# Performance work log

Measured on AMD Instinct MI355X. Metric: run time of the kernel, lower is better.

Reference implementation:

```python
import jax, jax.numpy as jnp
import numpy as np

NUM_HEADS = 16
NUM_KV_HEADS = 8
HEAD_DIM = 128
HIDDEN = 2048
Q_SIZE = NUM_HEADS * HEAD_DIM          # 2048
KV_SIZE = NUM_KV_HEADS * HEAD_DIM      # 1024
SCALING = 256.0 ** -0.5                # query_pre_attn_scalar ** -0.5
EPS = 1e-6
BATCH = 8
ENC_LEN = 512                          # encoder_len_per_req
Q_LEN = 2048                           # sum of extend_seq_lens (8 * 256)
KV_LEN = BATCH * ENC_LEN               # 4096


def _rms_norm(x, w):
    # Gemma3RMSNorm: fp32 compute, scale by (1 + weight)
    xf = x.astype(jnp.float32)
    xf = xf * jax.lax.rsqrt(jnp.mean(xf * xf, axis=-1, keepdims=True) + EPS)
    return (xf * (1.0 + w.astype(jnp.float32))).astype(x.dtype)


def setup_inputs() -> dict:
    key = jax.random.key(0)
    k1, k2, k3 = jax.random.split(key, 3)
    return {
        "hidden_states": jax.random.normal(k1, (Q_LEN, HIDDEN), jnp.float32),
        "encoder_hidden_states": jax.random.normal(k2, (KV_LEN, HIDDEN), jnp.float32),
        "w_qkv": jax.random.normal(k3, (Q_SIZE + 2 * KV_SIZE, HIDDEN), jnp.float32) * 0.02,
        "q_norm_w": jnp.zeros((HEAD_DIM,), jnp.float32),
        "k_norm_w": jnp.zeros((HEAD_DIM,), jnp.float32),
        "seq_lens": jnp.full((BATCH,), Q_LEN // BATCH, jnp.int32),  # extend_seq_lens per request
    }


def reference(hidden_states, encoder_hidden_states, w_qkv, q_norm_w, k_norm_w, seq_lens):
    # decoder side: only q is used
    qkv_dec = hidden_states @ w_qkv.T                     # [q_len, 4096]
    q = qkv_dec[:, :Q_SIZE].reshape(Q_LEN, NUM_HEADS, HEAD_DIM)
    q = _rms_norm(q, q_norm_w) * SCALING

    # encoder side: only k, v are used
    qkv_enc = encoder_hidden_states @ w_qkv.T             # [kv_len, 4096]
    k = qkv_enc[:, Q_SIZE:Q_SIZE + KV_SIZE].reshape(KV_LEN, NUM_KV_HEADS, HEAD_DIM)
    v = qkv_enc[:, Q_SIZE + KV_SIZE:].reshape(KV_LEN, NUM_KV_HEADS, HEAD_DIM)
    k = _rms_norm(k, k_norm_w)

    # GQA: repeat each kv head n_rep times (consecutively, matching expand+reshape)
    n_rep = NUM_HEADS // NUM_KV_HEADS
    k = jnp.repeat(k, n_rep, axis=1)                      # [kv_len, H, D]
    v = jnp.repeat(v, n_rep, axis=1)

    # scores per head: [H, q_len, kv_len]
    scores = jnp.einsum('qhd,khd->hqk', q, k)

    # ragged block-diagonal mask: query token i belongs to request r iff
    # cumsum(seq_lens)[r-1] <= i < cumsum(seq_lens)[r]; kv token j -> j // ENC_LEN
    q_req = jnp.searchsorted(jnp.cumsum(seq_lens), jnp.arange(Q_LEN), side='right')
    kv_req = jnp.arange(KV_LEN) // ENC_LEN
    mask = q_req[:, None] == kv_req[None, :]              # [q_len, kv_len] bool
    scores = jnp.where(mask[None, :, :], scores, -jnp.inf)

    attn = jax.nn.softmax(scores.astype(jnp.float32), axis=-1).astype(v.dtype)
    out = jnp.einsum('hqk,khd->qhd', attn, v)             # [q_len, H, D]
    return out.reshape(Q_LEN, NUM_HEADS * HEAD_DIM)
```

## Files before the change

kernel.cpp:

```cpp
#include <hip/hip_runtime.h>

typedef __attribute__((ext_vector_type(8))) short short8;
typedef __attribute__((ext_vector_type(4))) float f32x4;

#define DEVI __device__ __forceinline__

static constexpr int HIDDEN   = 2048;
static constexpr int NHEADS   = 16;
static constexpr int NKV      = 8;
static constexpr int HDIM     = 128;
static constexpr int QLEN     = 2048;
static constexpr int KVLEN    = 4096;
static constexpr int ENCLEN   = 512;
static constexpr int NREQ     = 8;
static constexpr float SCALING = 0.0625f;
static constexpr float EPS     = 1e-6f;

DEVI unsigned short f2bf(float f) {
  unsigned int b = __float_as_uint(f);
  b += 0x7FFFu + ((b >> 16) & 1u);
  return (unsigned short)(b >> 16);
}

DEVI void g2l16(const void* g, void* l) {
  __builtin_amdgcn_global_load_lds(
      (const __attribute__((address_space(1))) void*)g,
      (__attribute__((address_space(3))) void*)l, 16, 0, 0);
}

__global__ __launch_bounds__(256) void cvt_all(const float* __restrict__ h,
                                               const float* __restrict__ e,
                                               const float* __restrict__ w,
                                               unsigned short* __restrict__ hb,
                                               unsigned short* __restrict__ eb,
                                               unsigned short* __restrict__ wb) {
  constexpr long S1 = (long)2048 * 2048, S2 = (long)4096 * 2048;
  long i = ((long)blockIdx.x * 256 + threadIdx.x) * 8;
  const float* src;
  unsigned short* dst;
  if (i < S1)           { src = h + i;            dst = hb + i; }
  else if (i < S1 + S2) { src = e + (i - S1);     dst = eb + (i - S1); }
  else                  { src = w + (i - S1 - S2); dst = wb + (i - S1 - S2); }
  float4 a = *(const float4*)src;
  float4 b = *(const float4*)(src + 4);
  short8 o;
  o[0] = (short)f2bf(a.x); o[1] = (short)f2bf(a.y);
  o[2] = (short)f2bf(a.z); o[3] = (short)f2bf(a.w);
  o[4] = (short)f2bf(b.x); o[5] = (short)f2bf(b.y);
  o[6] = (short)f2bf(b.z); o[7] = (short)f2bf(b.w);
  *(short8*)dst = o;
}


#define SBAR  __builtin_amdgcn_s_barrier()

DEVI short8 rdfrag(const char* unit, int row, int lg) {
  int L = row >> 1;
  int g = ((row & 1) << 2) + lg;
  return *(const short8*)(unit + L * 128 + ((g ^ (L & 7)) << 4));
}

__global__ __launch_bounds__(512, 2) void gemm_qkv8(
    const unsigned short* __restrict__ Adec, const unsigned short* __restrict__ Aenc,
    const unsigned short* __restrict__ Bw,
    const float* __restrict__ q_nw, const float* __restrict__ k_nw,
    unsigned short* __restrict__ q_bf, unsigned short* __restrict__ k_bf,
    unsigned short* __restrict__ v_t) {
  extern __shared__ char lds[];
  const int K = 2048, NST = 64;

  int flat = blockIdx.y * 8 + blockIdx.x;
  int swz = (flat & 7) * 24 + (flat >> 3);
  int bx = swz & 7, by = swz >> 3;

  const unsigned short* A;
  int bm0;
  if (by < 8) { A = Adec; bm0 = by * 256; }
  else        { A = Aenc; bm0 = (by - 8) * 256; }
  const unsigned short* Bp = Bw + (by < 8 ? 0 : (size_t)2048 * 2048);
  const int bn0 = bx * 256;

  const int tid = threadIdx.x, lane = tid & 63, wave = tid >> 6;
  const int lr = lane & 15, lg = lane >> 4;
  const int wr = wave >> 2, wc = wave & 3;
  const int bq = (wc & 1) * 64;

  const int sB = tid * 16;
  const int sL = sB >> 7, sgp = (sB >> 4) & 7;
  const int sg = sgp ^ (sL & 7);
  const int st_row = sL * 2 + (sg >> 2);
  const int st_col = (sg & 3) * 8;
  const size_t a0off = (size_t)(bm0 + st_row) * K + st_col;
  const size_t a1off = a0off + (size_t)128 * K;
  const size_t b0off = (size_t)(bn0 + st_row) * K + st_col;
  const size_t b1off = b0off + (size_t)128 * K;

#define STG4(t)                                                       \
  {                                                                   \
    const size_t kc = (size_t)(t) * 32;                               \
    char* base = lds + ((t) % 3) * 32768;                             \
    g2l16(A + a0off + kc,  base + sB);                                \
    g2l16(A + a1off + kc,  base + 8192 + sB);                         \
    g2l16(Bp + b0off + kc, base + 16384 + sB);                        \
    g2l16(Bp + b1off + kc, base + 24576 + sB);                        \
  }

  f32x4 acc[8][4] = {};

#define MM(mq, aS, bS)                                                \
  {                                                                   \
    __builtin_amdgcn_s_setprio(1);                                    \
    _Pragma("unroll") for (int m = 0; m < 4; ++m)                     \
        _Pragma("unroll") for (int n = 0; n < 4; ++n)                 \
            acc[(mq)*4 + m][n] = __builtin_amdgcn_mfma_f32_16x16x32_bf16( \
                aS[m], bS[n], acc[(mq)*4 + m][n], 0, 0, 0);           \
    __builtin_amdgcn_s_setprio(0);                                    \
  }

  STG4(0); STG4(1);

#pragma unroll 3
  for (int t = 0; t < NST - 1; ++t) {
    asm volatile("s_waitcnt vmcnt(4)" ::: "memory");
    SBAR;
    const char* ua = lds + (t % 3) * 32768 + wr * 8192;
    const char* ub = lds + (t % 3) * 32768 + 16384 + ((wc >> 1) << 13);
    short8 a0[4], b0[4], a1[4];
#pragma unroll
    for (int m = 0; m < 4; ++m) a0[m] = rdfrag(ua, m * 16 + lr, lg);
#pragma unroll
    for (int n = 0; n < 4; ++n) b0[n] = rdfrag(ub, bq + n * 16 + lr, lg);
    if (t < NST - 2) STG4(t + 2);
    MM(0, a0, b0);
#pragma unroll
    for (int m = 0; m < 4; ++m) a1[m] = rdfrag(ua, 64 + m * 16 + lr, lg);
    MM(1, a1, b0);
  }
  {
    asm volatile("s_waitcnt vmcnt(0)" ::: "memory");
    SBAR;
    const char* ua = lds + ((NST - 1) % 3) * 32768 + wr * 8192;
    const char* ub = lds + ((NST - 1) % 3) * 32768 + 16384 + ((wc >> 1) << 13);
    short8 a0[4], b0[4], a1[4];
#pragma unroll
    for (int m = 0; m < 4; ++m) a0[m] = rdfrag(ua, m * 16 + lr, lg);
#pragma unroll
    for (int n = 0; n < 4; ++n) b0[n] = rdfrag(ub, bq + n * 16 + lr, lg);
    MM(0, a0, b0);
#pragma unroll
    for (int m = 0; m < 4; ++m) a1[m] = rdfrag(ua, 64 + m * 16 + lr, lg);
    MM(1, a1, b0);
  }

  const int btype = (by < 8) ? 0 : (bx < 4 ? 1 : 2);
  const int tokbase0 = (by < 8 ? by : by - 8) * 256;

  if (btype < 2) {
    float* Lf = (float*)lds;
    const float* wnorm = (btype == 0) ? q_nw : k_nw;
    const float fscale = (btype == 0) ? SCALING : 1.0f;
    unsigned short* dst = (btype == 0) ? q_bf : k_bf;
    const size_t LEN = (btype == 0) ? (size_t)QLEN : (size_t)KVLEN;
    const int dloc = lr * 8;
    float wv[8];
#pragma unroll
    for (int j = 0; j < 8; ++j) wv[j] = 1.0f + wnorm[dloc + j];

#pragma unroll
    for (int q = 0; q < 4; ++q) {
      SBAR;
      if (wr == (q >> 1)) {
        const int amb = (q & 1) * 4;
#pragma unroll
        for (int am2 = 0; am2 < 4; ++am2)
#pragma unroll
          for (int n = 0; n < 4; ++n)
#pragma unroll
            for (int r = 0; r < 4; ++r)
              Lf[(am2 * 16 + lg * 4 + r) * 260 + wc * 64 + n * 16 + lr] =
                  acc[amb + am2][n][r];
      }
      SBAR;
#pragma unroll
      for (int it = 0; it < 4; ++it) {
        int pair = it * 32 + wave * 4 + (lane >> 4);
        int row = pair >> 1, hh = pair & 1;
        const float* src = &Lf[row * 260 + hh * 128 + dloc];
        f32x4 x0 = *(const f32x4*)src;
        f32x4 x1 = *(const f32x4*)(src + 4);
        float ssq = x0[0]*x0[0] + x0[1]*x0[1] + x0[2]*x0[2] + x0[3]*x0[3] +
                    x1[0]*x1[0] + x1[1]*x1[1] + x1[2]*x1[2] + x1[3]*x1[3];
#pragma unroll
        for (int m = 8; m >= 1; m >>= 1) ssq += __shfl_xor(ssq, m);
        float sc = rsqrtf(ssq * (1.0f / 128.0f) + EPS) * fscale;
        short8 o;
        o[0] = (short)f2bf(x0[0] * sc * wv[0]); o[1] = (short)f2bf(x0[1] * sc * wv[1]);
        o[2] = (short)f2bf(x0[2] * sc * wv[2]); o[3] = (short)f2bf(x0[3] * sc * wv[3]);
        o[4] = (short)f2bf(x1[0] * sc * wv[4]); o[5] = (short)f2bf(x1[1] * sc * wv[5]);
        o[6] = (short)f2bf(x1[2] * sc * wv[6]); o[7] = (short)f2bf(x1[3] * sc * wv[7]);
        int tok = tokbase0 + q * 64 + row;
        int hd = 2 * bx + hh;
        *(short8*)&dst[((size_t)hd * LEN + tok) * 128 + dloc] = o;
      }
    }
  } else {
    float* Lv = (float*)lds;
#pragma unroll
    for (int q = 0; q < 4; ++q) {
      SBAR;
      if (wr == (q >> 1)) {
        const int amb = (q & 1) * 4;
#pragma unroll
        for (int am2 = 0; am2 < 4; ++am2)
#pragma unroll
          for (int n = 0; n < 4; ++n)
            *(f32x4*)&Lv[(wc * 64 + n * 16 + lr) * 68 + am2 * 16 + lg * 4] =
                acc[amb + am2][n];
      }
      SBAR;
      int d = tid >> 1, th = tid & 1;
      const float* src = &Lv[d * 68 + th * 32];
      int kh = (bx - 4) * 2 + (d >> 7);
      int tok = tokbase0 + q * 64 + th * 32;
      unsigned short* vp = &v_t[((size_t)kh * 128 + (d & 127)) * KVLEN + tok];
#pragma unroll
      for (int j = 0; j < 4; ++j) {
        f32x4 v0 = *(const f32x4*)(src + j * 8);
        f32x4 v1 = *(const f32x4*)(src + j * 8 + 4);
        short8 o;
        o[0] = (short)f2bf(v0[0]); o[1] = (short)f2bf(v0[1]);
        o[2] = (short)f2bf(v0[2]); o[3] = (short)f2bf(v0[3]);
        o[4] = (short)f2bf(v1[0]); o[5] = (short)f2bf(v1[1]);
        o[6] = (short)f2bf(v1[2]); o[7] = (short)f2bf(v1[3]);
        *(short8*)(vp + j * 8) = o;
      }
    }
  }
#undef STG4
#undef MM
}

__global__ __launch_bounds__(256, 4) void attn_kernel(
    const unsigned short* __restrict__ qb,
    const unsigned short* __restrict__ kb,
    const unsigned short* __restrict__ vt,
    const int* __restrict__ seq_lens,
    float* __restrict__ out) {
  __shared__ __align__(16) char smem[73728];

  const int h = blockIdx.y;
  const int t0 = blockIdx.x * 64;
  int req = 0, qs = 0;
#pragma unroll 1
  while (req < NREQ - 1 && qs + seq_lens[req] <= t0) { qs += seq_lens[req]; ++req; }
  const int slen = seq_lens[req];
  const int rows = min(64, qs + slen - t0);
  if (rows <= 0) return;
  const int qbase = t0;

  const int tid = threadIdx.x, lane = tid & 63, wave = tid >> 6;
  const int lr = lane & 15, lg = lane >> 4;
  const int m0w = wave * 16;
  const int kh = h >> 1;
  const int kv0 = req * ENCLEN;

#define STAGE_K(c, db)                                                        \
  _Pragma("unroll") for (int i = 0; i < 4; ++i) {                             \
    int idx = i * 256 + tid;                                                  \
    int row = idx >> 4, slot = idx & 15;                                      \
    g2l16(kb + ((size_t)kh * KVLEN + kv0 + (c) * 64 + row) * 128 +            \
              ((slot ^ (row & 15)) << 3),                                     \
          smem + (db) * 16384 + idx * 16);                                    \
  }
#define STAGE_V(c, db)                                                        \
  _Pragma("unroll") for (int i = 0; i < 4; ++i) {                             \
    int idx = i * 256 + tid;                                                  \
    int row = idx >> 3, slot = idx & 7;                                       \
    g2l16(vt + ((size_t)kh * 128 + row) * KVLEN + kv0 + (c) * 64 +            \
              ((slot ^ (row & 7)) << 3),                                      \
          smem + 32768 + (db) * 16384 + idx * 16);                            \
  }

  unsigned short* Ps = (unsigned short*)(smem + 65536);

  short8 a_q[4];
  {
    int qr = qbase + min(m0w + lr, rows - 1);
    const unsigned short* qp = qb + ((size_t)h * QLEN + qr) * 128 + lg * 8;
#pragma unroll
    for (int ks = 0; ks < 4; ++ks) a_q[ks] = *(const short8*)(qp + ks * 32);
  }

  f32x4 acc[8] = {};
  float mrow[4], lsum[4];
#pragma unroll
  for (int r = 0; r < 4; ++r) { mrow[r] = -1e30f; lsum[r] = 0.f; }

  STAGE_K(0, 0); STAGE_V(0, 0);

  int cb = 0;
#pragma unroll 1
  for (int c = 0; c < 8; ++c) {
    asm volatile("s_waitcnt vmcnt(0)" ::: "memory");
    __syncthreads();
    if (c < 7) { STAGE_K(c + 1, cb ^ 1); STAGE_V(c + 1, cb ^ 1); }
    const unsigned short* Kb = (const unsigned short*)(smem + cb * 16384);
    const unsigned short* Vb = (const unsigned short*)(smem + 32768 + cb * 16384);

    f32x4 s[4] = {};
#pragma unroll
    for (int ks = 0; ks < 4; ++ks) {
      short8 bk[4];
#pragma unroll
      for (int n = 0; n < 4; ++n) {
        int row = n * 16 + lr;
        bk[n] = *(const short8*)&Kb[row * 128 + (((ks * 4 + lg) ^ (row & 15)) << 3)];
      }
#pragma unroll
      for (int n = 0; n < 4; ++n)
        s[n] = __builtin_amdgcn_mfma_f32_16x16x32_bf16(a_q[ks], bk[n], s[n], 0, 0, 0);
    }

#pragma unroll
    for (int r = 0; r < 4; ++r) {
      float mx = fmaxf(fmaxf(s[0][r], s[1][r]), fmaxf(s[2][r], s[3][r]));
#pragma unroll
      for (int msk = 8; msk >= 1; msk >>= 1) mx = fmaxf(mx, __shfl_xor(mx, msk));
      float mnew = fmaxf(mrow[r], mx);
      float al = __expf(mrow[r] - mnew);
      mrow[r] = mnew;
      float rs = 0.f;
#pragma unroll
      for (int n = 0; n < 4; ++n) {
        float p = __expf(s[n][r] - mnew);
        s[n][r] = p;
        rs += p;
      }
#pragma unroll
      for (int msk = 8; msk >= 1; msk >>= 1) rs += __shfl_xor(rs, msk);
      lsum[r] = lsum[r] * al + rs;
#pragma unroll
      for (int n2 = 0; n2 < 8; ++n2) acc[n2][r] *= al;
    }

#pragma unroll
    for (int n = 0; n < 4; ++n)
#pragma unroll
      for (int r = 0; r < 4; ++r) {
        int row = m0w + lg * 4 + r;
        int col = n * 16 + lr;
        Ps[row * 64 + (col ^ ((row & 7) << 3))] = f2bf(s[n][r]);
      }
    asm volatile("s_waitcnt lgkmcnt(0)" ::: "memory");
    __builtin_amdgcn_sched_barrier(0);

#pragma unroll
    for (int ks = 0; ks < 2; ++ks) {
      int prow = m0w + lr;
      short8 pa = *(const short8*)&Ps[prow * 64 + (((ks * 4 + lg) ^ (prow & 7)) << 3)];
#pragma unroll
      for (int n2 = 0; n2 < 8; ++n2) {
        int row = n2 * 16 + lr;
        short8 bv = *(const short8*)&Vb[row * 64 + (((ks * 4 + lg) ^ (row & 7)) << 3)];
        acc[n2] = __builtin_amdgcn_mfma_f32_16x16x32_bf16(pa, bv, acc[n2], 0, 0, 0);
      }
    }
    cb ^= 1;
  }
  __syncthreads();

  float inv[4];
#pragma unroll
  for (int r = 0; r < 4; ++r) inv[r] = 1.0f / lsum[r];
#pragma unroll
  for (int n2 = 0; n2 < 8; ++n2)
#pragma unroll
    for (int r = 0; r < 4; ++r) acc[n2][r] *= inv[r];

  constexpr int OFS = 132;
  float* Of = (float*)smem;
#pragma unroll
  for (int n2 = 0; n2 < 8; ++n2)
#pragma unroll
    for (int r = 0; r < 4; ++r)
      Of[(m0w + lg * 4 + r) * OFS + n2 * 16 + lr] = acc[n2][r];
  __syncthreads();
#pragma unroll
  for (int p = 0; p < 8; ++p) {
    int idx = p * 256 + tid;
    int row = idx >> 5, c4 = (idx & 31) * 4;
    if (row < rows) {
      f32x4 v = *(const f32x4*)&Of[row * OFS + c4];
      *(f32x4*)&out[(size_t)(qbase + row) * 2048 + h * 128 + c4] = v;
    }
  }
#undef STAGE_K
#undef STAGE_V
}

extern "C" void kernel_launch(void* const* d_in, const int* in_sizes, int n_in,
                              void* d_out, int out_size, void* d_ws, size_t ws_size,
                              hipStream_t stream) {
  const float* hidden = (const float*)d_in[0];
  const float* enc    = (const float*)d_in[1];
  const float* w_qkv  = (const float*)d_in[2];
  const float* q_nw   = (const float*)d_in[3];
  const float* k_nw   = (const float*)d_in[4];
  const int*   slens  = (const int*)d_in[5];
  float* out = (float*)d_out;

  char* ws = (char*)d_ws;
  unsigned short* h_bf = (unsigned short*)(ws + 0);
  unsigned short* e_bf = (unsigned short*)(ws + 8388608);
  unsigned short* w_bf = (unsigned short*)(ws + 25165824);
  unsigned short* q_bf = (unsigned short*)(ws + 41943040);
  unsigned short* k_bf = (unsigned short*)(ws + 50331648);
  unsigned short* v_t  = (unsigned short*)(ws + 58720256);

  static bool attr_set = false;
  if (!attr_set) {
    hipFuncSetAttribute((const void*)gemm_qkv8,
                        hipFuncAttributeMaxDynamicSharedMemorySize, 131072);
    attr_set = true;
  }

  cvt_all<<<10240, 256, 0, stream>>>(hidden, enc, w_qkv, h_bf, e_bf, w_bf);

  gemm_qkv8<<<dim3(8, 24), 512, 131072, stream>>>(h_bf, e_bf, w_bf, q_nw, k_nw,
                                                  q_bf, k_bf, v_t);

  attn_kernel<<<dim3(32, 16), 256, 0, stream>>>(q_bf, k_bf, v_t, slens, out);
}
```

Before: 102.2 us.

## Shrink QKV GEMM tiles to 128x128 with 256-thread blocks for more parallelism

Reworks the fused QKV projection GEMM from 256x256 tiles with 512 threads to 128x128 tiles with 256 threads, launching 768 blocks instead of 192. Each block now maps to exactly one head, which simplifies the RMS-norm and V-transpose epilogues. The aim is to fill all CUs and allow more resident blocks per CU, at the cost of reloading operands more often from global memory and lower arithmetic intensity per block.

```diff
diff --git a/kernel.cpp b/kernel.cpp
--- a/kernel.cpp
+++ b/kernel.cpp
@@ -60,7 +60,7 @@
   return *(const short8*)(unit + L * 128 + ((g ^ (L & 7)) << 4));
 }
 
-__global__ __launch_bounds__(512, 2) void gemm_qkv8(
+__global__ __launch_bounds__(256, 3) void gemm_qkv8(
     const unsigned short* __restrict__ Adec, const unsigned short* __restrict__ Aenc,
     const unsigned short* __restrict__ Bw,
     const float* __restrict__ q_nw, const float* __restrict__ k_nw,
@@ -69,51 +69,55 @@
   extern __shared__ char lds[];
   const int K = 2048, NST = 64;
 
-  int flat = blockIdx.y * 8 + blockIdx.x;
-  int swz = (flat & 7) * 24 + (flat >> 3);
-  int bx = swz & 7, by = swz >> 3;
+  int flat = blockIdx.x;
+  int swz = (flat & 7) * 96 + (flat >> 3);
+  int bx = swz / 48, byy = swz % 48;
 
   const unsigned short* A;
   int bm0;
-  if (by < 8) { A = Adec; bm0 = by * 256; }
-  else        { A = Aenc; bm0 = (by - 8) * 256; }
-  const unsigned short* Bp = Bw + (by < 8 ? 0 : (size_t)2048 * 2048);
-  const int bn0 = bx * 256;
+  if (byy < 16) { A = Adec; bm0 = byy * 128; }
+  else          { A = Aenc; bm0 = (byy - 16) * 128; }
+  const unsigned short* Bp = Bw + (byy < 16 ? 0 : (size_t)2048 * 2048);
+  const int bn0 = bx * 128;
 
   const int tid = threadIdx.x, lane = tid & 63, wave = tid >> 6;
   const int lr = lane & 15, lg = lane >> 4;
-  const int wr = wave >> 2, wc = wave & 3;
-  const int bq = (wc & 1) * 64;
-
-  const int sB = tid * 16;
-  const int sL = sB >> 7, sgp = (sB >> 4) & 7;
-  const int sg = sgp ^ (sL & 7);
-  const int st_row = sL * 2 + (sg >> 2);
-  const int st_col = (sg & 3) * 8;
-  const size_t a0off = (size_t)(bm0 + st_row) * K + st_col;
-  const size_t a1off = a0off + (size_t)128 * K;
-  const size_t b0off = (size_t)(bn0 + st_row) * K + st_col;
-  const size_t b1off = b0off + (size_t)128 * K;
+  const int wr = wave >> 1, wc = wave & 1;
+
+  int srow[2], scol[2];
+#pragma unroll
+  for (int i = 0; i < 2; ++i) {
+    int sB = (i * 256 + tid) * 16;
+    int sL = sB >> 7, sgp = (sB >> 4) & 7;
+    int sg = sgp ^ (sL & 7);
+    srow[i] = sL * 2 + (sg >> 2);
+    scol[i] = (sg & 3) * 8;
+  }
+  const size_t aoff0 = (size_t)(bm0 + srow[0]) * K + scol[0];
+  const size_t aoff1 = (size_t)(bm0 + srow[1]) * K + scol[1];
+  const size_t boff0 = (size_t)(bn0 + srow[0]) * K + scol[0];
+  const size_t boff1 = (size_t)(bn0 + srow[1]) * K + scol[1];
+  const int dB = tid * 16;
 
 #define STG4(t)                                                       \
   {                                                                   \
     const size_t kc = (size_t)(t) * 32;                               \
-    char* base = lds + ((t) % 3) * 32768;                             \
-    g2l16(A + a0off + kc,  base + sB);                                \
-    g2l16(A + a1off + kc,  base + 8192 + sB);                         \
-    g2l16(Bp + b0off + kc, base + 16384 + sB);                        \
-    g2l16(Bp + b1off + kc, base + 24576 + sB);                        \
-  }
-
-  f32x4 acc[8][4] = {};
-
-#define MM(mq, aS, bS)                                                \
+    char* base = lds + ((t) % 3) * 16384;                             \
+    g2l16(A + aoff0 + kc,  base + dB);                                \
+    g2l16(A + aoff1 + kc,  base + 4096 + dB);                         \
+    g2l16(Bp + boff0 + kc, base + 8192 + dB);                         \
+    g2l16(Bp + boff1 + kc, base + 12288 + dB);                        \
+  }
+
+  f32x4 acc[4][4] = {};
+
+#define MM16(aS, bS)                                                  \
   {                                                                   \
     __builtin_amdgcn_s_setprio(1);                                    \
     _Pragma("unroll") for (int m = 0; m < 4; ++m)                     \
         _Pragma("unroll") for (int n = 0; n < 4; ++n)                 \
-            acc[(mq)*4 + m][n] = __builtin_amdgcn_mfma_f32_16x16x32_bf16( \
-                aS[m], bS[n], acc[(mq)*4 + m][n], 0, 0, 0);           \
+            acc[m][n] = __builtin_amdgcn_mfma_f32_16x16x32_bf16(      \
+                aS[m], bS[n], acc[m][n], 0, 0, 0);                    \
     __builtin_amdgcn_s_setprio(0);                                    \
   }
 
@@ -123,37 +127,30 @@
   for (int t = 0; t < NST - 1; ++t) {
     asm volatile("s_waitcnt vmcnt(4)" ::: "memory");
     SBAR;
-    const char* ua = lds + (t % 3) * 32768 + wr * 8192;
-    const char* ub = lds + (t % 3) * 32768 + 16384 + ((wc >> 1) << 13);
-    short8 a0[4], b0[4], a1[4];
-#pragma unroll
-    for (int m = 0; m < 4; ++m) a0[m] = rdfrag(ua, m * 16 + lr, lg);
-#pragma unroll
-    for (int n = 0; n < 4; ++n) b0[n] = rdfrag(ub, bq + n * 16 + lr, lg);
+    const char* ua = lds + (t % 3) * 16384;
+    const char* ub = ua + 8192;
+    short8 a[4], b[4];
+#pragma unroll
+    for (int m = 0; m < 4; ++m) a[m] = rdfrag(ua, wr * 64 + m * 16 + lr, lg);
+#pragma unroll
+    for (int n = 0; n < 4; ++n) b[n] = rdfrag(ub, wc * 64 + n * 16 + lr, lg);
     if (t < NST - 2) STG4(t + 2);
-    MM(0, a0, b0);
-#pragma unroll
-    for (int m = 0; m < 4; ++m) a1[m] = rdfrag(ua, 64 + m * 16 + lr, lg);
-    MM(1, a1, b0);
+    MM16(a, b);
   }
   {
     asm volatile("s_waitcnt vmcnt(0)" ::: "memory");
     SBAR;
-    const char* ua = lds + ((NST - 1) % 3) * 32768 + wr * 8192;
-    const char* ub = lds + ((NST - 1) % 3) * 32768 + 16384 + ((wc >> 1) << 13);
-    short8 a0[4], b0[4], a1[4];
-#pragma unroll
-    for (int m = 0; m < 4; ++m) a0[m] = rdfrag(ua, m * 16 + lr, lg);
-#pragma unroll
-    for (int n = 0; n < 4; ++n) b0[n] = rdfrag(ub, bq + n * 16 + lr, lg);
-    MM(0, a0, b0);
-#pragma unroll
-    for (int m = 0; m < 4; ++m) a1[m] = rdfrag(ua, 64 + m * 16 + lr, lg);
-    MM(1, a1, b0);
-  }
-
-  const int btype = (by < 8) ? 0 : (bx < 4 ? 1 : 2);
-  const int tokbase0 = (by < 8 ? by : by - 8) * 256;
+    const char* ua = lds + ((NST - 1) % 3) * 16384;
+    const char* ub = ua + 8192;
+    short8 a[4], b[4];
+#pragma unroll
+    for (int m = 0; m < 4; ++m) a[m] = rdfrag(ua, wr * 64 + m * 16 + lr, lg);
+#pragma unroll
+    for (int n = 0; n < 4; ++n) b[n] = rdfrag(ub, wc * 64 + n * 16 + lr, lg);
+    MM16(a, b);
+  }
+
+  const int btype = (byy < 16) ? 0 : (bx < 8 ? 1 : 2);
 
   if (btype < 2) {
     float* Lf = (float*)lds;
@@ -161,68 +158,65 @@
     const float fscale = (btype == 0) ? SCALING : 1.0f;
     unsigned short* dst = (btype == 0) ? q_bf : k_bf;
     const size_t LEN = (btype == 0) ? (size_t)QLEN : (size_t)KVLEN;
-    const int dloc = lr * 8;
+    const int g16 = tid >> 4, l16 = tid & 15;
+    const int dloc = l16 * 8;
     float wv[8];
 #pragma unroll
     for (int j = 0; j < 8; ++j) wv[j] = 1.0f + wnorm[dloc + j];
 
 #pragma unroll
-    for (int q = 0; q < 4; ++q) {
+    for (int hh = 0; hh < 2; ++hh) {
       SBAR;
-      if (wr == (q >> 1)) {
-        const int amb = (q & 1) * 4;
-#pragma unroll
-        for (int am2 = 0; am2 < 4; ++am2)
+      if (wr == hh) {
+#pragma unroll
+        for (int m = 0; m < 4; ++m)
 #pragma unroll
           for (int n = 0; n < 4; ++n)
 #pragma unroll
             for (int r = 0; r < 4; ++r)
-              Lf[(am2 * 16 + lg * 4 + r) * 260 + wc * 64 + n * 16 + lr] =
-                  acc[amb + am2][n][r];
+              Lf[(m * 16 + lg * 4 + r) * 132 + wc * 64 + n * 16 + lr] =
+                  acc[m][n][r];
       }
       SBAR;
 #pragma unroll
       for (int it = 0; it < 4; ++it) {
-        int pair = it * 32 + wave * 4 + (lane >> 4);
-        int row = pair >> 1, hh = pair & 1;
-        const float* src = &Lf[row * 260 + hh * 128 + dloc];
+        int row = it * 16 + g16;
+        const float* src = &Lf[row * 132 + dloc];
         f32x4 x0 = *(const f32x4*)src;
         f32x4 x1 = *(const f32x4*)(src + 4);
         float ssq = x0[0]*x0[0] + x0[1]*x0[1] + x0[2]*x0[2] + x0[3]*x0[3] +
                     x1[0]*x1[0] + x1[1]*x1[1] + x1[2]*x1[2] + x1[3]*x1[3];
 #pragma unroll
-        for (int m = 8; m >= 1; m >>= 1) ssq += __shfl_xor(ssq, m);
+        for (int msk = 8; msk >= 1; msk >>= 1) ssq += __shfl_xor(ssq, msk);
         float sc = rsqrtf(ssq * (1.0f / 128.0f) + EPS) * fscale;
         short8 o;
         o[0] = (short)f2bf(x0[0] * sc * wv[0]); o[1] = (short)f2bf(x0[1] * sc * wv[1]);
         o[2] = (short)f2bf(x0[2] * sc * wv[2]); o[3] = (short)f2bf(x0[3] * sc * wv[3]);
         o[4] = (short)f2bf(x1[0] * sc * wv[4]); o[5] = (short)f2bf(x1[1] * sc * wv[5]);
         o[6] = (short)f2bf(x1[2] * sc * wv[6]); o[7] = (short)f2bf(x1[3] * sc * wv[7]);
-        int tok = tokbase0 + q * 64 + row;
-        int hd = 2 * bx + hh;
-        *(short8*)&dst[((size_t)hd * LEN + tok) * 128 + dloc] = o;
+        int tok = bm0 + hh * 64 + row;
+        *(short8*)&dst[((size_t)bx * LEN + tok) * 128 + dloc] = o;
       }
     }
   } else {
     float* Lv = (float*)lds;
-#pragma unroll
-    for (int q = 0; q < 4; ++q) {
+    const int kh = bx - 8;
+#pragma unroll
+    for (int hh = 0; hh < 2; ++hh) {
       SBAR;
-      if (wr == (q >> 1)) {
-        const int amb = (q & 1) * 4;
-#pragma unroll
-        for (int am2 = 0; am2 < 4; ++am2)
+      if (wr == hh) {
+#pragma unroll
+        for (int m = 0; m < 4; ++m)
 #pragma unroll
           for (int n = 0; n < 4; ++n)
-            *(f32x4*)&Lv[(wc * 64 + n * 16 + lr) * 68 + am2 * 16 + lg * 4] =
-                acc[amb + am2][n];
+            *(f32x4*)&Lv[(wc * 64 + n * 16 + lr) * 66 + m * 16 + lg * 4] =
+                acc[m][n];
       }
       SBAR;
       int d = tid >> 1, th = tid & 1;
-      const float* src = &Lv[d * 68 + th * 32];
-      int kh = (bx - 4) * 2 + (d >> 7);
-      int tok = tokbase0 + q * 64 + th * 32;
-      unsigned short* vp = &v_t[((size_t)kh * 128 + (d & 127)) * KVLEN + tok];
+      const float* src = &Lv[d * 66 + th * 32];
+      int tok0 = bm0 + hh * 64 + th * 32;
+      unsigned short* vp = &v_t[((size_t)kh * 128 + d) * KVLEN + tok0];
 #pragma unroll
       for (int j = 0; j < 4; ++j) {
         f32x4 v0 = *(const f32x4*)(src + j * 8);
@@ -237,7 +231,7 @@
     }
   }
 #undef STG4
-#undef MM
+#undef MM16
 }
 
 __global__ __launch_bounds__(256, 4) void attn_kernel(
@@ -420,14 +414,14 @@
   static bool attr_set = false;
   if (!attr_set) {
     hipFuncSetAttribute((const void*)gemm_qkv8,
-                        hipFuncAttributeMaxDynamicSharedMemorySize, 131072);
+                        hipFuncAttributeMaxDynamicSharedMemorySize, 49152);
     attr_set = true;
   }
 
   cvt_all<<<10240, 256, 0, stream>>>(hidden, enc, w_qkv, h_bf, e_bf, w_bf);
 
-  gemm_qkv8<<<dim3(8, 24), 512, 131072, stream>>>(h_bf, e_bf, w_bf, q_nw, k_nw,
-                                                  q_bf, k_bf, v_t);
+  gemm_qkv8<<<768, 256, 49152, stream>>>(h_bf, e_bf, w_bf, q_nw, k_nw,
+                                         q_bf, k_bf, v_t);
 
   attn_kernel<<<dim3(32, 16), 256, 0, stream>>>(q_bf, k_bf, v_t, slens, out);
 }
```

Result: slower. 118.0 us (+15.4%).

## Fuse fp32-to-bf16 conversion into QKV GEMM staging and drop separate convert kernel

Applied to the files above, without the earlier changes.

Removes the standalone cvt_all kernel and has the GEMM load fp32 activations and weights straight into registers, convert them with v_cvt_pk_bf16_f32, and write bf16 tiles into LDS. The staging changes from asynchronous global-to-LDS loads to register-staged loads issued one iteration ahead and written after the MFMAs, with an lgkmcnt wait and barrier. This avoids writing and re-reading the bf16 copies and one launch. The costs are twice the global read bytes per tile inside the GEMM, more register pressure, and re-converting each fp32 element every time a tile is reloaded.

```diff
diff --git a/kernel.cpp b/kernel.cpp
--- a/kernel.cpp
+++ b/kernel.cpp
@@ -22,37 +22,21 @@
   return (unsigned short)(b >> 16);
 }
 
+DEVI unsigned cvtpk(float lo, float hi) {
+  unsigned r;
+  asm("v_cvt_pk_bf16_f32 %0, %1, %2" : "=v"(r) : "v"(lo), "v"(hi));
+  return r;
+}
+
 DEVI void g2l16(const void* g, void* l) {
   __builtin_amdgcn_global_load_lds(
       (const __attribute__((address_space(1))) void*)g,
       (__attribute__((address_space(3))) void*)l, 16, 0, 0);
 }
 
-__global__ __launch_bounds__(256) void cvt_all(const float* __restrict__ h,
-                                               const float* __restrict__ e,
-                                               const float* __restrict__ w,
-                                               unsigned short* __restrict__ hb,
-                                               unsigned short* __restrict__ eb,
-                                               unsigned short* __restrict__ wb) {
-  constexpr long S1 = (long)2048 * 2048, S2 = (long)4096 * 2048;
-  long i = ((long)blockIdx.x * 256 + threadIdx.x) * 8;
-  const float* src;
-  unsigned short* dst;
-  if (i < S1)           { src = h + i;            dst = hb + i; }
-  else if (i < S1 + S2) { src = e + (i - S1);     dst = eb + (i - S1); }
-  else                  { src = w + (i - S1 - S2); dst = wb + (i - S1 - S2); }
-  float4 a = *(const float4*)src;
-  float4 b = *(const float4*)(src + 4);
-  short8 o;
-  o[0] = (short)f2bf(a.x); o[1] = (short)f2bf(a.y);
-  o[2] = (short)f2bf(a.z); o[3] = (short)f2bf(a.w);
-  o[4] = (short)f2bf(b.x); o[5] = (short)f2bf(b.y);
-  o[6] = (short)f2bf(b.z); o[7] = (short)f2bf(b.w);
-  *(short8*)dst = o;
-}
-
 
 #define SBAR  __builtin_amdgcn_s_barrier()
+#define LGKMB { asm volatile("s_waitcnt lgkmcnt(0)" ::: "memory"); }
 
 DEVI short8 rdfrag(const char* unit, int row, int lg) {
   int L = row >> 1;
@@ -61,8 +45,8 @@
 }
 
 __global__ __launch_bounds__(512, 2) void gemm_qkv8(
-    const unsigned short* __restrict__ Adec, const unsigned short* __restrict__ Aenc,
-    const unsigned short* __restrict__ Bw,
+    const float* __restrict__ Adec, const float* __restrict__ Aenc,
+    const float* __restrict__ Ww,
     const float* __restrict__ q_nw, const float* __restrict__ k_nw,
     unsigned short* __restrict__ q_bf, unsigned short* __restrict__ k_bf,
     unsigned short* __restrict__ v_t) {
@@ -73,11 +57,11 @@
   int swz = (flat & 7) * 24 + (flat >> 3);
   int bx = swz & 7, by = swz >> 3;
 
-  const unsigned short* A;
+  const float* A;
   int bm0;
   if (by < 8) { A = Adec; bm0 = by * 256; }
   else        { A = Aenc; bm0 = (by - 8) * 256; }
-  const unsigned short* Bp = Bw + (by < 8 ? 0 : (size_t)2048 * 2048);
+  const float* Bp = Ww + (by < 8 ? 0 : (size_t)2048 * 2048);
   const int bn0 = bx * 256;
 
   const int tid = threadIdx.x, lane = tid & 63, wave = tid >> 6;
@@ -95,16 +79,6 @@
   const size_t b0off = (size_t)(bn0 + st_row) * K + st_col;
   const size_t b1off = b0off + (size_t)128 * K;
 
-#define STG4(t)                                                       \
-  {                                                                   \
-    const size_t kc = (size_t)(t) * 32;                               \
-    char* base = lds + ((t) % 3) * 32768;                             \
-    g2l16(A + a0off + kc,  base + sB);                                \
-    g2l16(A + a1off + kc,  base + 8192 + sB);                         \
-    g2l16(Bp + b0off + kc, base + 16384 + sB);                        \
-    g2l16(Bp + b1off + kc, base + 24576 + sB);                        \
-  }
-
   f32x4 acc[8][4] = {};
 
 #define MM(mq, aS, bS)                                                \
@@ -117,12 +91,42 @@
     __builtin_amdgcn_s_setprio(0);                                    \
   }
 
-  STG4(0); STG4(1);
+#define STAGE_LOAD(t, R)                                              \
+  {                                                                   \
+    const size_t kc = (size_t)(t) * 32;                               \
+    R[0] = *(const f32x4*)(A + a0off + kc);                           \
+    R[1] = *(const f32x4*)(A + a0off + kc + 4);                       \
+    R[2] = *(const f32x4*)(A + a1off + kc);                           \
+    R[3] = *(const f32x4*)(A + a1off + kc + 4);                       \
+    R[4] = *(const f32x4*)(Bp + b0off + kc);                          \
+    R[5] = *(const f32x4*)(Bp + b0off + kc + 4);                      \
+    R[6] = *(const f32x4*)(Bp + b1off + kc);                          \
+    R[7] = *(const f32x4*)(Bp + b1off + kc + 4);                      \
+  }
+#define STAGE_WRITE(t, R)                                             \
+  {                                                                   \
+    char* base = lds + ((t) % 3) * 32768;                             \
+    _Pragma("unroll") for (int u = 0; u < 4; ++u) {                   \
+      unsigned w0 = cvtpk(R[u * 2][0], R[u * 2][1]);                  \
+      unsigned w1 = cvtpk(R[u * 2][2], R[u * 2][3]);                  \
+      unsigned w2 = cvtpk(R[u * 2 + 1][0], R[u * 2 + 1][1]);          \
+      unsigned w3 = cvtpk(R[u * 2 + 1][2], R[u * 2 + 1][3]);          \
+      uint4 pk = make_uint4(w0, w1, w2, w3);                          \
+      *(uint4*)(base + u * 8192 + sB) = pk;                           \
+    }                                                                 \
+  }
+
+  {
+    f32x4 R[8];
+    STAGE_LOAD(0, R); STAGE_WRITE(0, R);
+    STAGE_LOAD(1, R); STAGE_WRITE(1, R);
+  }
+  LGKMB; SBAR;
 
 #pragma unroll 3
   for (int t = 0; t < NST - 1; ++t) {
-    asm volatile("s_waitcnt vmcnt(4)" ::: "memory");
-    SBAR;
+    f32x4 R[8];
+    if (t < NST - 2) STAGE_LOAD(t + 2, R);
     const char* ua = lds + (t % 3) * 32768 + wr * 8192;
     const char* ub = lds + (t % 3) * 32768 + 16384 + ((wc >> 1) << 13);
     short8 a0[4], b0[4], a1[4];
@@ -130,15 +134,14 @@
     for (int m = 0; m < 4; ++m) a0[m] = rdfrag(ua, m * 16 + lr, lg);
 #pragma unroll
     for (int n = 0; n < 4; ++n) b0[n] = rdfrag(ub, bq + n * 16 + lr, lg);
-    if (t < NST - 2) STG4(t + 2);
     MM(0, a0, b0);
 #pragma unroll
     for (int m = 0; m < 4; ++m) a1[m] = rdfrag(ua, 64 + m * 16 + lr, lg);
     MM(1, a1, b0);
+    if (t < NST - 2) STAGE_WRITE(t + 2, R);
+    LGKMB; SBAR;
   }
   {
-    asm volatile("s_waitcnt vmcnt(0)" ::: "memory");
-    SBAR;
     const char* ua = lds + ((NST - 1) % 3) * 32768 + wr * 8192;
     const char* ub = lds + ((NST - 1) % 3) * 32768 + 16384 + ((wc >> 1) << 13);
     short8 a0[4], b0[4], a1[4];
@@ -236,8 +239,9 @@
       }
     }
   }
-#undef STG4
 #undef MM
+#undef STAGE_LOAD
+#undef STAGE_WRITE
 }
 
 __global__ __launch_bounds__(256, 4) void attn_kernel(
@@ -410,12 +414,9 @@
   float* out = (float*)d_out;
 
   char* ws = (char*)d_ws;
-  unsigned short* h_bf = (unsigned short*)(ws + 0);
-  unsigned short* e_bf = (unsigned short*)(ws + 8388608);
-  unsigned short* w_bf = (unsigned short*)(ws + 25165824);
-  unsigned short* q_bf = (unsigned short*)(ws + 41943040);
-  unsigned short* k_bf = (unsigned short*)(ws + 50331648);
-  unsigned short* v_t  = (unsigned short*)(ws + 58720256);
+  unsigned short* q_bf = (unsigned short*)(ws + 0);
+  unsigned short* k_bf = (unsigned short*)(ws + 8388608);
+  unsigned short* v_t  = (unsigned short*)(ws + 16777216);
 
   static bool attr_set = false;
   if (!attr_set) {
@@ -424,9 +425,7 @@
     attr_set = true;
   }
 
-  cvt_all<<<10240, 256, 0, stream>>>(hidden, enc, w_qkv, h_bf, e_bf, w_bf);
-
-  gemm_qkv8<<<dim3(8, 24), 512, 131072, stream>>>(h_bf, e_bf, w_bf, q_nw, k_nw,
+  gemm_qkv8<<<dim3(8, 24), 512, 131072, stream>>>(hidden, enc, w_qkv, q_nw, k_nw,
                                                   q_bf, k_bf, v_t);
 
   attn_kernel<<<dim3(32, 16), 256, 0, stream>>>(q_bf, k_bf, v_t, slens, out);
```

Result: slower. 105.0 us (+2.7%).

## Restructure QKV GEMM main loop to double-buffered 64-wide K tiles

Applied to the files above, without the earlier changes.

Replaces the triple-buffered 32-wide K pipeline (64 stages, prefetch two ahead) with a double-buffered 64-wide K tile pipeline (32 stages). Each stage runs four quadrant MFMA phases separated by barriers, and the LDS layout becomes a row-major 128-byte row with an XOR swizzle. The goal is fewer loop iterations and more MFMA work per staged tile. In exchange, LDS use grows to 128KB per block, which may cut occupancy below the two blocks the launch bounds ask for. It also adds many extra barriers and a full vmcnt(0) wait each iteration, which can stall the pipeline.

```diff
diff --git a/kernel.cpp b/kernel.cpp
--- a/kernel.cpp
+++ b/kernel.cpp
@@ -54,10 +54,8 @@
 
 #define SBAR  __builtin_amdgcn_s_barrier()
 
-DEVI short8 rdfrag(const char* unit, int row, int lg) {
-  int L = row >> 1;
-  int g = ((row & 1) << 2) + lg;
-  return *(const short8*)(unit + L * 128 + ((g ^ (L & 7)) << 4));
+DEVI short8 rdfrag(const char* half, int row, int g) {
+  return *(const short8*)(half + row * 128 + ((g ^ (row & 7)) << 4));
 }
 
 __global__ __launch_bounds__(512, 2) void gemm_qkv8(
@@ -67,7 +65,7 @@
     unsigned short* __restrict__ q_bf, unsigned short* __restrict__ k_bf,
     unsigned short* __restrict__ v_t) {
   extern __shared__ char lds[];
-  const int K = 2048, NST = 64;
+  const int K = 2048, NKT = 32;
 
   int flat = blockIdx.y * 8 + blockIdx.x;
   int swz = (flat & 7) * 24 + (flat >> 3);
@@ -83,73 +81,75 @@
   const int tid = threadIdx.x, lane = tid & 63, wave = tid >> 6;
   const int lr = lane & 15, lg = lane >> 4;
   const int wr = wave >> 2, wc = wave & 3;
-  const int bq = (wc & 1) * 64;
-
-  const int sB = tid * 16;
-  const int sL = sB >> 7, sgp = (sB >> 4) & 7;
-  const int sg = sgp ^ (sL & 7);
-  const int st_row = sL * 2 + (sg >> 2);
-  const int st_col = (sg & 3) * 8;
-  const size_t a0off = (size_t)(bm0 + st_row) * K + st_col;
-  const size_t a1off = a0off + (size_t)128 * K;
-  const size_t b0off = (size_t)(bn0 + st_row) * K + st_col;
-  const size_t b1off = b0off + (size_t)128 * K;
-
-#define STG4(t)                                                       \
-  {                                                                   \
-    const size_t kc = (size_t)(t) * 32;                               \
-    char* base = lds + ((t) % 3) * 32768;                             \
-    g2l16(A + a0off + kc,  base + sB);                                \
-    g2l16(A + a1off + kc,  base + 8192 + sB);                         \
-    g2l16(Bp + b0off + kc, base + 16384 + sB);                        \
-    g2l16(Bp + b1off + kc, base + 24576 + sB);                        \
+  const int bcol0 = (wc & 1) * 64;
+
+#define AH(b, h) (lds + (b) * 65536 + (h) * 16384)
+#define BH(b, h) (lds + (b) * 65536 + 32768 + (h) * 16384)
+
+  int srow[2], scol[2];
+#pragma unroll
+  for (int i = 0; i < 2; ++i) {
+    int c = i * 512 + tid;
+    srow[i] = c >> 3;
+    scol[i] = ((c & 7) ^ ((c >> 3) & 7)) * 8;
+  }
+
+#define STG_KT(kt)                                                            \
+  {                                                                           \
+    const int b_ = (kt) & 1;                                                  \
+    const size_t kb_ = (size_t)(kt) * 64;                                     \
+    _Pragma("unroll") for (int i = 0; i < 2; ++i) {                           \
+      const int d_ = (i * 512 + tid) * 16;                                    \
+      g2l16(A  + (size_t)(bm0 + srow[i]) * K + kb_ + scol[i],       AH(b_, 0) + d_); \
+      g2l16(A  + (size_t)(bm0 + 128 + srow[i]) * K + kb_ + scol[i], AH(b_, 1) + d_); \
+      g2l16(Bp + (size_t)(bn0 + srow[i]) * K + kb_ + scol[i],       BH(b_, 0) + d_); \
+      g2l16(Bp + (size_t)(bn0 + 128 + srow[i]) * K + kb_ + scol[i], BH(b_, 1) + d_); \
+    }                                                                         \
   }
 
   f32x4 acc[8][4] = {};
-
-#define MM(mq, aS, bS)                                                \
-  {                                                                   \
-    __builtin_amdgcn_s_setprio(1);                                    \
-    _Pragma("unroll") for (int m = 0; m < 4; ++m)                     \
-        _Pragma("unroll") for (int n = 0; n < 4; ++n)                 \
-            acc[(mq)*4 + m][n] = __builtin_amdgcn_mfma_f32_16x16x32_bf16( \
-                aS[m], bS[n], acc[(mq)*4 + m][n], 0, 0, 0);           \
-    __builtin_amdgcn_s_setprio(0);                                    \
-  }
-
-  STG4(0); STG4(1);
-
-#pragma unroll 3
-  for (int t = 0; t < NST - 1; ++t) {
-    asm volatile("s_waitcnt vmcnt(4)" ::: "memory");
+  short8 a[4][2], b[2][2];
+
+#define LOAD_A(buf, qm)                                                       \
+  {                                                                           \
+    const char* ah = AH(buf, wr);                                             \
+    _Pragma("unroll") for (int m = 0; m < 4; ++m)                             \
+        _Pragma("unroll") for (int kk = 0; kk < 2; ++kk)                      \
+            a[m][kk] = rdfrag(ah, (qm) * 64 + m * 16 + lr, kk * 4 + lg);      \
+  }
+#define LOAD_B(buf, qn)                                                       \
+  {                                                                           \
+    const char* bh = BH(buf, wc >> 1);                                        \
+    _Pragma("unroll") for (int n = 0; n < 2; ++n)                             \
+        _Pragma("unroll") for (int kk = 0; kk < 2; ++kk)                      \
+            b[n][kk] = rdfrag(bh, bcol0 + (qn) * 32 + n * 16 + lr, kk * 4 + lg); \
+  }
+#define MM16(qm, qn)                                                          \
+  {                                                                           \
+    __builtin_amdgcn_s_setprio(1);                                            \
+    _Pragma("unroll") for (int m = 0; m < 4; ++m)                             \
+        _Pragma("unroll") for (int n = 0; n < 2; ++n)                         \
+            _Pragma("unroll") for (int kk = 0; kk < 2; ++kk)                  \
+                acc[(qm)*4 + m][(qn)*2 + n] =                                 \
+                    __builtin_amdgcn_mfma_f32_16x16x32_bf16(                  \
+                        a[m][kk], b[n][kk], acc[(qm)*4 + m][(qn)*2 + n], 0, 0, 0); \
+    __builtin_amdgcn_s_setprio(0);                                            \
+  }
+
+  STG_KT(0);
+  asm volatile("s_waitcnt vmcnt(0)" ::: "memory");
+  SBAR;
+
+#pragma unroll 2
+  for (int kt = 0; kt < NKT; ++kt) {
+    const int cb = kt & 1;
+    if (kt + 1 < NKT) STG_KT(kt + 1);
+    LOAD_A(cb, 0); LOAD_B(cb, 0); SBAR; MM16(0, 0); SBAR;
+    LOAD_B(cb, 1);                SBAR; MM16(0, 1); SBAR;
+    LOAD_A(cb, 1); LOAD_B(cb, 0); SBAR; MM16(1, 0); SBAR;
+    LOAD_B(cb, 1);                SBAR; MM16(1, 1);
+    if (kt + 1 < NKT) asm volatile("s_waitcnt vmcnt(0)" ::: "memory");
     SBAR;
-    const char* ua = lds + (t % 3) * 32768 + wr * 8192;
-    const char* ub = lds + (t % 3) * 32768 + 16384 + ((wc >> 1) << 13);
-    short8 a0[4], b0[4], a1[4];
-#pragma unroll
-    for (int m = 0; m < 4; ++m) a0[m] = rdfrag(ua, m * 16 + lr, lg);
-#pragma unroll
-    for (int n = 0; n < 4; ++n) b0[n] = rdfrag(ub, bq + n * 16 + lr, lg);
-    if (t < NST - 2) STG4(t + 2);
-    MM(0, a0, b0);
-#pragma unroll
-    for (int m = 0; m < 4; ++m) a1[m] = rdfrag(ua, 64 + m * 16 + lr, lg);
-    MM(1, a1, b0);
-  }
-  {
-    asm volatile("s_waitcnt vmcnt(0)" ::: "memory");
-    SBAR;
-    const char* ua = lds + ((NST - 1) % 3) * 32768 + wr * 8192;
-    const char* ub = lds + ((NST - 1) % 3) * 32768 + 16384 + ((wc >> 1) << 13);
-    short8 a0[4], b0[4], a1[4];
-#pragma unroll
-    for (int m = 0; m < 4; ++m) a0[m] = rdfrag(ua, m * 16 + lr, lg);
-#pragma unroll
-    for (int n = 0; n < 4; ++n) b0[n] = rdfrag(ub, bq + n * 16 + lr, lg);
-    MM(0, a0, b0);
-#pragma unroll
-    for (int m = 0; m < 4; ++m) a1[m] = rdfrag(ua, 64 + m * 16 + lr, lg);
-    MM(1, a1, b0);
   }
 
   const int btype = (by < 8) ? 0 : (bx < 4 ? 1 : 2);
@@ -236,8 +236,12 @@
       }
     }
   }
-#undef STG4
-#undef MM
+#undef AH
+#undef BH
+#undef STG_KT
+#undef LOAD_A
+#undef LOAD_B
+#undef MM16
 }
 
 __global__ __launch_bounds__(256, 4) void attn_kernel(
```

New measurement: 114.4 us. +11.9%, slower.
